# Kernel optimization log

Hardware: AMD Instinct MI355X
Metric: run time of the kernel (lower is better)

Reference implementation:

```python
import jax, jax.numpy as jnp
import numpy as np

B, C, H, W = 8, 64, 16, 16
TE = 128      # te_hidden
GT = 256      # rn_gt_hidden
FP = 256      # rn_fp_hidden
A = 32        # a_size
O = H * W
PAIR_IN = (C + 2) * 2 + TE  # 260, matches (cv_filter+2)*2 + te_hidden


def setup_inputs() -> dict:
    key = jax.random.key(0)
    ks = jax.random.split(key, 10)

    def w(k, fan_in, fan_out):
        return (jax.random.normal(k, (fan_in, fan_out), jnp.float32)
                / np.sqrt(fan_in).astype(np.float32))

    return {
        "x": jax.random.normal(ks[0], (B, C, H, W), jnp.float32),
        "code": jax.random.normal(ks[1], (B, TE), jnp.float32),
        "gt_w1": w(ks[2], PAIR_IN, GT), "gt_b1": jnp.zeros((GT,), jnp.float32),
        "gt_w2": w(ks[3], GT, GT),      "gt_b2": jnp.zeros((GT,), jnp.float32),
        "gt_w3": w(ks[4], GT, GT),      "gt_b3": jnp.zeros((GT,), jnp.float32),
        "fp_w1": w(ks[5], GT, FP),      "fp_b1": jnp.zeros((FP,), jnp.float32),
        "fp_w2": w(ks[6], FP, FP),      "fp_b2": jnp.zeros((FP,), jnp.float32),
        "fp_w3": w(ks[7], FP, A),       "fp_b3": jnp.zeros((A,), jnp.float32),
    }


def _coords(h, w):
    # 2 normalized coordinate channels in [-1, 1], one value per object
    ys = jnp.linspace(-1.0, 1.0, h, dtype=jnp.float32)
    xs = jnp.linspace(-1.0, 1.0, w, dtype=jnp.float32)
    yy, xx = jnp.meshgrid(ys, xs, indexing="ij")
    return jnp.stack([yy.ravel(), xx.ravel()], axis=-1)  # (o, 2)


def reference(x, code, gt_w1, gt_b1, gt_w2, gt_b2, gt_w3, gt_b3,
              fp_w1, fp_b1, fp_w2, fp_b2, fp_w3, fp_b3):
    b, c, h, w = x.shape
    o = h * w
    te = code.shape[-1]

    # rn_encode: flatten spatial grid to objects, append 2 coord channels
    xo = x.reshape(b, c, o).transpose(0, 2, 1)                 # (b, o, c)
    coord = jnp.broadcast_to(_coords(h, w)[None], (b, o, 2))
    xo = jnp.concatenate([xo, coord], axis=-1)                 # (b, o, c+2)

    # all O^2 ordered pairs + broadcast question code
    xi = jnp.broadcast_to(xo[:, :, None, :], (b, o, o, c + 2))
    xj = jnp.broadcast_to(xo[:, None, :, :], (b, o, o, c + 2))
    q = jnp.broadcast_to(code[:, None, None, :], (b, o, o, te))
    pairs = jnp.concatenate([xi, xj, q], axis=-1)              # (b, o, o, PAIR_IN)

    # g_theta MLP (ReLU after every layer)
    h1 = jax.nn.relu(pairs @ gt_w1 + gt_b1)
    h2 = jax.nn.relu(h1 @ gt_w2 + gt_b2)
    rel = jax.nn.relu(h2 @ gt_w3 + gt_b3)                      # (b, o, o, GT)

    # lower_sum: sum relations over the lower-triangular (i >= j) pairs
    mask = jnp.tril(jnp.ones((o, o), rel.dtype))
    summed = jnp.einsum("bijd,ij->bd", rel, mask)              # (b, GT)

    # f_phi MLP; no activation on final logits, dropout=0 (eval)
    f1 = jax.nn.relu(summed @ fp_w1 + fp_b1)
    f2 = jax.nn.relu(f1 @ fp_w2 + fp_b2)
    logits = f2 @ fp_w3 + fp_b3                                # (b, A)
    return logits
```

## Files before the change

kernel.cpp:

```cpp
#include <hip/hip_runtime.h>
#include <stdint.h>


#define NPAIR 32896

using short8  = __attribute__((ext_vector_type(8))) short;
using float4v = __attribute__((ext_vector_type(4))) float;

__device__ __forceinline__ float asf(unsigned u) {
    union { unsigned u; float f; } c; c.u = u; return c.f;
}
__device__ __forceinline__ unsigned short f2bf(float f) {
    union { float f; unsigned u; } c; c.f = f;
    unsigned u = c.u;
    u += 0x7FFFu + ((u >> 16) & 1u);
    return (unsigned short)(u >> 16);
}
__device__ __forceinline__ unsigned cvtpk(float lo, float hi) {
    unsigned r;
    asm("v_cvt_pk_bf16_f32 %0, %1, %2" : "=v"(r) : "v"(lo), "v"(hi));
    return r;
}
__device__ __forceinline__ void ij_of(int p, int& i, int& j) {
    float s = sqrtf(8.0f * (float)p + 1.0f);
    i = (int)((s - 1.0f) * 0.5f);
    while ((i + 1) * (i + 2) / 2 <= p) ++i;
    while (i * (i + 1) / 2 > p) --i;
    j = p - i * (i + 1) / 2;
}
__device__ __forceinline__ short8 buildA(uint4 uu, uint4 vv) {
    unsigned ua[4] = {uu.x, uu.y, uu.z, uu.w};
    unsigned va[4] = {vv.x, vv.y, vv.z, vv.w};
    union { unsigned u[4]; short8 s; } c;
    #pragma unroll
    for (int q = 0; q < 4; ++q) {
        float lo = asf(ua[q] << 16)         + asf(va[q] << 16);
        float hi = asf(ua[q] & 0xFFFF0000u) + asf(va[q] & 0xFFFF0000u);
        c.u[q] = cvtpk(fmaxf(lo, 0.f), fmaxf(hi, 0.f));
    }
    return c.s;
}

__global__ __launch_bounds__(256) void k_pre(
    const float* __restrict__ x, const float* __restrict__ code,
    const float* __restrict__ w1, const float* __restrict__ b1,
    const float* __restrict__ w2, const float* __restrict__ w3,
    unsigned short* __restrict__ ub, unsigned short* __restrict__ vb,
    unsigned short* __restrict__ w2t, unsigned short* __restrict__ w3t,
    float* __restrict__ summed)
{
    const int tid = threadIdx.x;
    if (blockIdx.x < 32) {
        const int ig = blockIdx.x, b = blockIdx.y, d = tid;
        float q = b1[d];
        const float* cp = code + b * 128;
        #pragma unroll 16
        for (int t = 0; t < 128; ++t) q += cp[t] * w1[(132 + t) * 256 + d];
        float su[8], sv[8];
        #pragma unroll
        for (int k = 0; k < 8; ++k) { su[k] = q; sv[k] = 0.f; }
        const float* xp = x + (b * 64) * 256 + ig * 8;
        #pragma unroll 8
        for (int c = 0; c < 64; ++c) {
            const float wu = w1[c * 256 + d];
            const float wv = w1[(66 + c) * 256 + d];
            const float* xc = xp + c * 256;
            #pragma unroll
            for (int k = 0; k < 8; ++k) { su[k] += xc[k] * wu; sv[k] += xc[k] * wv; }
        }
        const float wyu = w1[64 * 256 + d],  wxu = w1[65 * 256 + d];
        const float wyv = w1[130 * 256 + d], wxv = w1[131 * 256 + d];
        #pragma unroll
        for (int k = 0; k < 8; ++k) {
            const int i = ig * 8 + k;
            const float yy = (float)(i >> 4) * (2.0f / 15.0f) - 1.0f;
            const float xx = (float)(i & 15) * (2.0f / 15.0f) - 1.0f;
            ub[(b * 256 + i) * 256 + d] = f2bf(su[k] + yy * wyu + xx * wxu);
            vb[(b * 256 + i) * 256 + d] = f2bf(sv[k] + yy * wyv + xx * wxv);
        }
    } else {
        __shared__ float t[64][65];
        const int y = blockIdx.y;
        summed[y * 256 + tid] = 0.f;
        const int tx = tid & 63, ty = tid >> 6;
        for (int jj = 0; jj < 4; ++jj) {
            const int job = y * 4 + jj;
            const float* src = (job & 16) ? w3 : w2;
            unsigned short* dst = (job & 16) ? w3t : w2t;
            const int k0 = ((job >> 2) & 3) * 64, n0 = (job & 3) * 64;
            __syncthreads();
            #pragma unroll
            for (int r = ty; r < 64; r += 4) t[r][tx] = src[(k0 + r) * 256 + n0 + tx];
            __syncthreads();
            #pragma unroll
            for (int r = ty; r < 64; r += 4) dst[(n0 + r) * 256 + k0 + tx] = f2bf(t[tx][r]);
        }
    }
}

__global__ __launch_bounds__(512) void k_fuse(
    const unsigned short* __restrict__ ub, const unsigned short* __restrict__ vb,
    const unsigned short* __restrict__ w2t, const unsigned short* __restrict__ w3t,
    const float* __restrict__ b2, const float* __restrict__ b3,
    float* __restrict__ summed)
{
    extern __shared__ unsigned short lds[];
    const int tid  = threadIdx.x;
    const int pt   = blockIdx.x, b = blockIdx.y;
    const int lane = tid & 63, w = tid >> 6;
    const int lm   = lane & 15, quad = lane >> 4;

    #pragma unroll
    for (int it = 0; it < 16; ++it) {
        const int idx = it * 512 + tid;
        const int n = idx >> 5, c = idx & 31;
        const uint4 d = *(const uint4*)(w2t + n * 256 + c * 8);
        *(uint4*)(&lds[n * 256 + ((c ^ (n & 7)) << 3)]) = d;
    }

    const unsigned short* up[2];
    const unsigned short* vp[2];
    #pragma unroll
    for (int mt = 0; mt < 2; ++mt) {
        const int p = pt * 256 + w * 32 + mt * 16 + lm;
        int i, j; ij_of(p, i, j);
        up[mt] = ub + ((b * 256 + i) * 256) + quad * 8;
        vp[mt] = vb + ((b * 256 + j) * 256) + quad * 8;
    }
    __syncthreads();

    const float4v zero4 = {0.f, 0.f, 0.f, 0.f};

    float4v acc1[16][2];
    #pragma unroll
    for (int nt = 0; nt < 16; ++nt)
        #pragma unroll
        for (int mt = 0; mt < 2; ++mt) acc1[nt][mt] = zero4;
    {
        uint4 cu[3][2], cv[3][2];
        #pragma unroll
        for (int kk = 0; kk < 3; ++kk)
            #pragma unroll
            for (int mt = 0; mt < 2; ++mt) {
                cu[kk][mt] = *(const uint4*)(up[mt] + kk * 32);
                cv[kk][mt] = *(const uint4*)(vp[mt] + kk * 32);
            }
        #pragma unroll
        for (int ks = 0; ks < 8; ++ks) {
            const int pr = ks % 3;
            short8 afr[2];
            #pragma unroll
            for (int mt = 0; mt < 2; ++mt) afr[mt] = buildA(cu[pr][mt], cv[pr][mt]);
            if (ks < 5) {
                #pragma unroll
                for (int mt = 0; mt < 2; ++mt) {
                    cu[pr][mt] = *(const uint4*)(up[mt] + (ks + 3) * 32);
                    cv[pr][mt] = *(const uint4*)(vp[mt] + (ks + 3) * 32);
                }
            }
            const int coff = ((ks * 4 + quad) ^ (lm & 7)) << 3;
            __builtin_amdgcn_s_setprio(1);
            #pragma unroll
            for (int ng = 0; ng < 4; ++ng) {
                short8 bfr[4];
                #pragma unroll
                for (int q = 0; q < 4; ++q)
                    bfr[q] = *(const short8*)(&lds[((ng * 4 + q) * 16 + lm) * 256 + coff]);
                #pragma unroll
                for (int q = 0; q < 4; ++q)
                    #pragma unroll
                    for (int mt = 0; mt < 2; ++mt)
                        acc1[ng * 4 + q][mt] = __builtin_amdgcn_mfma_f32_16x16x32_bf16(
                            bfr[q], afr[mt], acc1[ng * 4 + q][mt], 0, 0, 0);
            }
            __builtin_amdgcn_s_setprio(0);
        }
    }
    __syncthreads();

    const unsigned short* bb3 = w3t + ((w * 32 + lm) * 256) + quad * 8;
    short8 bbuf[2][2];
    #pragma unroll
    for (int kk = 0; kk < 2; ++kk)
        #pragma unroll
        for (int nt = 0; nt < 2; ++nt)
            bbuf[kk][nt] = *(const short8*)(bb3 + nt * 4096 + kk * 32);

    #pragma unroll
    for (int nt = 0; nt < 16; ++nt) {
        const float4 bbv = *(const float4*)(b2 + nt * 16 + quad * 4);
        #pragma unroll
        for (int mt = 0; mt < 2; ++mt) {
            const int row = w * 32 + mt * 16 + lm;
            const float v0 = fmaxf(acc1[nt][mt][0] + bbv.x, 0.f);
            const float v1 = fmaxf(acc1[nt][mt][1] + bbv.y, 0.f);
            const float v2 = fmaxf(acc1[nt][mt][2] + bbv.z, 0.f);
            const float v3 = fmaxf(acc1[nt][mt][3] + bbv.w, 0.f);
            uint2 pk; pk.x = cvtpk(v0, v1); pk.y = cvtpk(v2, v3);
            const int c0 = nt * 2 + (quad >> 1);
            *(uint2*)(&lds[row * 256 + (((c0 ^ (row & 7)) << 3) | ((quad & 1) << 2))]) = pk;
        }
    }
    __syncthreads();

    float4v acc2[16][2];
    #pragma unroll
    for (int mt = 0; mt < 16; ++mt)
        #pragma unroll
        for (int nt = 0; nt < 2; ++nt) acc2[mt][nt] = zero4;
    {
        for (int ks = 0; ks < 8; ++ks) {
            const int pr = ks & 1;
            short8 bcur[2];
            #pragma unroll
            for (int nt = 0; nt < 2; ++nt) bcur[nt] = bbuf[pr][nt];
            if (ks < 6) {
                #pragma unroll
                for (int nt = 0; nt < 2; ++nt)
                    bbuf[pr][nt] = *(const short8*)(bb3 + nt * 4096 + (ks + 2) * 32);
            }
            __builtin_amdgcn_s_setprio(1);
            #pragma unroll
            for (int mt = 0; mt < 16; ++mt) {
                const int row = mt * 16 + lm;
                const short8 a = *(const short8*)(
                    &lds[row * 256 + (((ks * 4 + quad) ^ (row & 7)) << 3)]);
                #pragma unroll
                for (int nt = 0; nt < 2; ++nt)
                    acc2[mt][nt] = __builtin_amdgcn_mfma_f32_16x16x32_bf16(
                        a, bcur[nt], acc2[mt][nt], 0, 0, 0);
            }
            __builtin_amdgcn_s_setprio(0);
        }
    }

    #pragma unroll
    for (int nt = 0; nt < 2; ++nt) {
        const int col = w * 32 + nt * 16 + lm;
        const float bb = b3[col];
        float s = 0.f;
        #pragma unroll
        for (int mt = 0; mt < 16; ++mt)
            #pragma unroll
            for (int rg = 0; rg < 4; ++rg)
                s += fmaxf(acc2[mt][nt][rg] + bb, 0.f);
        s += __shfl_xor(s, 16);
        s += __shfl_xor(s, 32);
        if (quad == 0)
            atomicAdd(&summed[b * 256 + col], s);
    }
}

__global__ __launch_bounds__(1024) void k_tail(
    const unsigned short* __restrict__ ub, const unsigned short* __restrict__ vb,
    const unsigned short* __restrict__ w2t, const unsigned short* __restrict__ w3t,
    const float* __restrict__ b2, const float* __restrict__ b3,
    const float* __restrict__ summed,
    const float* __restrict__ fw1, const float* __restrict__ fb1,
    const float* __restrict__ fw2, const float* __restrict__ fb2,
    const float* __restrict__ fw3, const float* __restrict__ fb3,
    float* __restrict__ out)
{
    extern __shared__ unsigned short lds[];
    float* ext = (float*)(lds + 65536);
    float* s0  = ext + 256;
    float* s1  = s0 + 256;
    float* red = s1 + 256;
    const int b = blockIdx.x, tid = threadIdx.x;
    const int lane = tid & 63, w = tid >> 6;
    const int lm = lane & 15, quad = lane >> 4;
    const float4v zero4 = {0.f, 0.f, 0.f, 0.f};

    #pragma unroll
    for (int it = 0; it < 8; ++it) {
        const int idx = it * 1024 + tid;
        const int n = idx >> 5, c = idx & 31;
        const uint4 d4 = *(const uint4*)(w2t + n * 256 + c * 8);
        *(uint4*)(&lds[n * 256 + ((c ^ (n & 7)) << 3)]) = d4;
    }
    const int pp = 32768 + w * 16 + lm;
    const int p  = pp < NPAIR ? pp : NPAIR - 1;
    int i, j; ij_of(p, i, j);
    const unsigned short* up = ub + ((b * 256 + i) * 256) + quad * 8;
    const unsigned short* vp = vb + ((b * 256 + j) * 256) + quad * 8;
    __syncthreads();

    float4v acc1[16];
    #pragma unroll
    for (int nt = 0; nt < 16; ++nt) acc1[nt] = zero4;
    if (tid < 512) {
        #pragma unroll
        for (int ks = 0; ks < 8; ++ks) {
            const uint4 cu = *(const uint4*)(up + ks * 32);
            const uint4 cv = *(const uint4*)(vp + ks * 32);
            const short8 afr = buildA(cu, cv);
            const int coff = ((ks * 4 + quad) ^ (lm & 7)) << 3;
            #pragma unroll
            for (int nt = 0; nt < 16; ++nt) {
                const short8 bfr = *(const short8*)(&lds[(nt * 16 + lm) * 256 + coff]);
                acc1[nt] = __builtin_amdgcn_mfma_f32_16x16x32_bf16(
                    bfr, afr, acc1[nt], 0, 0, 0);
            }
        }
    }
    __syncthreads();

    if (tid < 512) {
        #pragma unroll
        for (int nt = 0; nt < 16; ++nt) {
            const float4 bbv = *(const float4*)(b2 + nt * 16 + quad * 4);
            const int row = w * 16 + lm;
            const float v0 = fmaxf(acc1[nt][0] + bbv.x, 0.f);
            const float v1 = fmaxf(acc1[nt][1] + bbv.y, 0.f);
            const float v2 = fmaxf(acc1[nt][2] + bbv.z, 0.f);
            const float v3 = fmaxf(acc1[nt][3] + bbv.w, 0.f);
            uint2 pk; pk.x = cvtpk(v0, v1); pk.y = cvtpk(v2, v3);
            const int c0 = nt * 2 + (quad >> 1);
            *(uint2*)(&lds[row * 256 + (((c0 ^ (row & 7)) << 3) | ((quad & 1) << 2))]) = pk;
        }
    }
    __syncthreads();

    float4v acc2[8][2];
    #pragma unroll
    for (int mt = 0; mt < 8; ++mt)
        #pragma unroll
        for (int nt = 0; nt < 2; ++nt) acc2[mt][nt] = zero4;
    if (tid < 512) {
        const unsigned short* bb3 = w3t + ((w * 32 + lm) * 256) + quad * 8;
        #pragma unroll
        for (int ks = 0; ks < 8; ++ks) {
            short8 bcur[2];
            #pragma unroll
            for (int nt = 0; nt < 2; ++nt)
                bcur[nt] = *(const short8*)(bb3 + nt * 4096 + ks * 32);
            const int coff = ((ks * 4 + quad) ^ (lm & 7)) << 3;
            #pragma unroll
            for (int mt = 0; mt < 8; ++mt) {
                const int row = mt * 16 + lm;
                const short8 a = *(const short8*)(
                    &lds[row * 256 + (((ks * 4 + quad) ^ (row & 7)) << 3)]);
                #pragma unroll
                for (int nt = 0; nt < 2; ++nt)
                    acc2[mt][nt] = __builtin_amdgcn_mfma_f32_16x16x32_bf16(
                        a, bcur[nt], acc2[mt][nt], 0, 0, 0);
            }
        }
        #pragma unroll
        for (int nt = 0; nt < 2; ++nt) {
            const int col = w * 32 + nt * 16 + lm;
            const float bb = b3[col];
            float s = 0.f;
            #pragma unroll
            for (int mt = 0; mt < 8; ++mt)
                #pragma unroll
                for (int rg = 0; rg < 4; ++rg)
                    s += fmaxf(acc2[mt][nt][rg] + bb, 0.f);
            s += __shfl_xor(s, 16);
            s += __shfl_xor(s, 32);
            if (quad == 0) ext[col] = s;
        }
    }
    __syncthreads();

    const int d = tid & 255, kh = tid >> 8;
    if (tid < 256) s0[tid] = summed[b * 256 + tid] + ext[tid];
    __syncthreads();
    float pk = 0.f;
    #pragma unroll 16
    for (int k = kh * 64; k < kh * 64 + 64; ++k) pk += s0[k] * fw1[k * 256 + d];
    red[kh * 256 + d] = pk;
    __syncthreads();
    if (tid < 256)
        s1[tid] = fmaxf(red[tid] + red[256 + tid] + red[512 + tid] + red[768 + tid]
                        + fb1[tid], 0.f);
    __syncthreads();
    pk = 0.f;
    #pragma unroll 16
    for (int k = kh * 64; k < kh * 64 + 64; ++k) pk += s1[k] * fw2[k * 256 + d];
    red[kh * 256 + d] = pk;
    __syncthreads();
    if (tid < 256)
        s0[tid] = fmaxf(red[tid] + red[256 + tid] + red[512 + tid] + red[768 + tid]
                        + fb2[tid], 0.f);
    __syncthreads();
    const int d3 = tid & 31, kh3 = tid >> 5;
    pk = 0.f;
    #pragma unroll
    for (int k = kh3 * 8; k < kh3 * 8 + 8; ++k) pk += s0[k] * fw3[k * 32 + d3];
    red[kh3 * 32 + d3] = pk;
    __syncthreads();
    if (tid < 32) {
        float o = fb3[tid];
        #pragma unroll 8
        for (int r = 0; r < 32; ++r) o += red[r * 32 + tid];
        out[b * 32 + tid] = o;
    }
}

extern "C" void kernel_launch(void* const* d_in, const int* in_sizes, int n_in,
                              void* d_out, int out_size, void* d_ws, size_t ws_size,
                              hipStream_t stream) {
    const float* x    = (const float*)d_in[0];
    const float* code = (const float*)d_in[1];
    const float* gw1  = (const float*)d_in[2];
    const float* gb1  = (const float*)d_in[3];
    const float* gw2  = (const float*)d_in[4];
    const float* gb2  = (const float*)d_in[5];
    const float* gw3  = (const float*)d_in[6];
    const float* gb3  = (const float*)d_in[7];
    const float* fw1  = (const float*)d_in[8];
    const float* fb1  = (const float*)d_in[9];
    const float* fw2  = (const float*)d_in[10];
    const float* fb2  = (const float*)d_in[11];
    const float* fw3  = (const float*)d_in[12];
    const float* fb3  = (const float*)d_in[13];
    float* out = (float*)d_out;

    char* ws = (char*)d_ws;
    unsigned short* ub  = (unsigned short*)(ws);
    unsigned short* vb  = (unsigned short*)(ws + 1048576);
    unsigned short* w2t = (unsigned short*)(ws + 2097152);
    unsigned short* w3t = (unsigned short*)(ws + 2228224);
    float* summed = (float*)(ws + 2359296);

    hipLaunchKernelGGL(k_pre, dim3(33, 8), dim3(256), 0, stream,
                       x, code, gw1, gb1, gw2, gw3, ub, vb, w2t, w3t, summed);
    hipLaunchKernelGGL(k_fuse, dim3(128, 8), dim3(512), 131072, stream,
                       ub, vb, w2t, w3t, gb2, gb3, summed);
    hipLaunchKernelGGL(k_tail, dim3(8), dim3(1024), 138240, stream,
                       ub, vb, w2t, w3t, gb2, gb3, summed,
                       fw1, fb1, fw2, fb2, fw3, fb3, out);
}
```

Baseline: 187.7 us.

## Stage built pair activations in LDS and use 2x4 warp tiling for both GEMMs

Layer-1 pair activations (relu(u_i+v_j)) are now built once per block and written to swizzled LDS, instead of being recomputed in registers per warp. W2 is no longer staged in LDS; its fragments are streamed from global memory with double buffering, as W3 already was. Warps are arranged as a 2x4 grid (128 rows by 64 columns per warp) for both the layer-2 and layer-3 MFMA GEMMs. This raises fragment reuse in registers and cuts LDS traffic per MFMA, at the cost of more global/L2 reads of weights per block and different register pressure. An unused coff variable is removed from k_tail.

```diff
diff --git a/kernel.cpp b/kernel.cpp
--- a/kernel.cpp
+++ b/kernel.cpp
@@ -39,6 +39,11 @@
         c.u[q] = cvtpk(fmaxf(lo, 0.f), fmaxf(hi, 0.f));
     }
     return c.s;
+}
+__device__ __forceinline__ uint4 build4(uint4 uu, uint4 vv) {
+    union { uint4 v; short8 s; } c;
+    c.s = buildA(uu, vv);
+    return c.v;
 }
 
 __global__ __launch_bounds__(256) void k_pre(
@@ -108,125 +113,119 @@
     const int tid  = threadIdx.x;
     const int pt   = blockIdx.x, b = blockIdx.y;
     const int lane = tid & 63, w = tid >> 6;
+    const int wm   = w >> 2, wn = w & 3;
     const int lm   = lane & 15, quad = lane >> 4;
 
-    #pragma unroll
-    for (int it = 0; it < 16; ++it) {
-        const int idx = it * 512 + tid;
-        const int n = idx >> 5, c = idx & 31;
-        const uint4 d = *(const uint4*)(w2t + n * 256 + c * 8);
-        *(uint4*)(&lds[n * 256 + ((c ^ (n & 7)) << 3)]) = d;
-    }
-
-    const unsigned short* up[2];
-    const unsigned short* vp[2];
-    #pragma unroll
-    for (int mt = 0; mt < 2; ++mt) {
-        const int p = pt * 256 + w * 32 + mt * 16 + lm;
+    const unsigned short* bb2 = w2t + ((wn * 64 + lm) * 256) + quad * 8;
+    const unsigned short* bb3 = w3t + ((wn * 64 + lm) * 256) + quad * 8;
+
+    short8 bbuf[2][4];
+    #pragma unroll
+    for (int kk = 0; kk < 2; ++kk)
+        #pragma unroll
+        for (int nt = 0; nt < 4; ++nt)
+            bbuf[kk][nt] = *(const short8*)(bb2 + nt * 4096 + kk * 32);
+
+    {
+        const int r = tid >> 1, half = tid & 1;
+        const int p = pt * 256 + r;
         int i, j; ij_of(p, i, j);
-        up[mt] = ub + ((b * 256 + i) * 256) + quad * 8;
-        vp[mt] = vb + ((b * 256 + j) * 256) + quad * 8;
+        const unsigned short* up = ub + ((b * 256 + i) * 256) + half * 128;
+        const unsigned short* vp = vb + ((b * 256 + j) * 256) + half * 128;
+        const int rs = r & 7;
+        #pragma unroll
+        for (int it = 0; it < 16; ++it) {
+            const uint4 uu = *(const uint4*)(up + it * 8);
+            const uint4 vv = *(const uint4*)(vp + it * 8);
+            const uint4 r4 = build4(uu, vv);
+            const int chunk = half * 16 + it;
+            *(uint4*)(&lds[r * 256 + ((chunk ^ rs) << 3)]) = r4;
+        }
     }
     __syncthreads();
 
     const float4v zero4 = {0.f, 0.f, 0.f, 0.f};
 
-    float4v acc1[16][2];
-    #pragma unroll
-    for (int nt = 0; nt < 16; ++nt)
-        #pragma unroll
-        for (int mt = 0; mt < 2; ++mt) acc1[nt][mt] = zero4;
+    float4v acc1[4][8];
+    #pragma unroll
+    for (int nt = 0; nt < 4; ++nt)
+        #pragma unroll
+        for (int mt = 0; mt < 8; ++mt) acc1[nt][mt] = zero4;
     {
-        uint4 cu[3][2], cv[3][2];
-        #pragma unroll
-        for (int kk = 0; kk < 3; ++kk)
-            #pragma unroll
-            for (int mt = 0; mt < 2; ++mt) {
-                cu[kk][mt] = *(const uint4*)(up[mt] + kk * 32);
-                cv[kk][mt] = *(const uint4*)(vp[mt] + kk * 32);
-            }
-        #pragma unroll
         for (int ks = 0; ks < 8; ++ks) {
-            const int pr = ks % 3;
-            short8 afr[2];
-            #pragma unroll
-            for (int mt = 0; mt < 2; ++mt) afr[mt] = buildA(cu[pr][mt], cv[pr][mt]);
-            if (ks < 5) {
-                #pragma unroll
-                for (int mt = 0; mt < 2; ++mt) {
-                    cu[pr][mt] = *(const uint4*)(up[mt] + (ks + 3) * 32);
-                    cv[pr][mt] = *(const uint4*)(vp[mt] + (ks + 3) * 32);
-                }
+            const int pr = ks & 1;
+            short8 bcur[4];
+            #pragma unroll
+            for (int nt = 0; nt < 4; ++nt) bcur[nt] = bbuf[pr][nt];
+            if (ks < 6) {
+                #pragma unroll
+                for (int nt = 0; nt < 4; ++nt)
+                    bbuf[pr][nt] = *(const short8*)(bb2 + nt * 4096 + (ks + 2) * 32);
             }
             const int coff = ((ks * 4 + quad) ^ (lm & 7)) << 3;
             __builtin_amdgcn_s_setprio(1);
             #pragma unroll
-            for (int ng = 0; ng < 4; ++ng) {
-                short8 bfr[4];
-                #pragma unroll
-                for (int q = 0; q < 4; ++q)
-                    bfr[q] = *(const short8*)(&lds[((ng * 4 + q) * 16 + lm) * 256 + coff]);
-                #pragma unroll
-                for (int q = 0; q < 4; ++q)
-                    #pragma unroll
-                    for (int mt = 0; mt < 2; ++mt)
-                        acc1[ng * 4 + q][mt] = __builtin_amdgcn_mfma_f32_16x16x32_bf16(
-                            bfr[q], afr[mt], acc1[ng * 4 + q][mt], 0, 0, 0);
+            for (int mt = 0; mt < 8; ++mt) {
+                const short8 afr = *(const short8*)(
+                    &lds[(wm * 128 + mt * 16 + lm) * 256 + coff]);
+                #pragma unroll
+                for (int nt = 0; nt < 4; ++nt)
+                    acc1[nt][mt] = __builtin_amdgcn_mfma_f32_16x16x32_bf16(
+                        bcur[nt], afr, acc1[nt][mt], 0, 0, 0);
             }
             __builtin_amdgcn_s_setprio(0);
         }
     }
     __syncthreads();
 
-    const unsigned short* bb3 = w3t + ((w * 32 + lm) * 256) + quad * 8;
-    short8 bbuf[2][2];
     #pragma unroll
     for (int kk = 0; kk < 2; ++kk)
         #pragma unroll
-        for (int nt = 0; nt < 2; ++nt)
+        for (int nt = 0; nt < 4; ++nt)
             bbuf[kk][nt] = *(const short8*)(bb3 + nt * 4096 + kk * 32);
 
     #pragma unroll
-    for (int nt = 0; nt < 16; ++nt) {
-        const float4 bbv = *(const float4*)(b2 + nt * 16 + quad * 4);
-        #pragma unroll
-        for (int mt = 0; mt < 2; ++mt) {
-            const int row = w * 32 + mt * 16 + lm;
+    for (int nt = 0; nt < 4; ++nt) {
+        const float4 bbv = *(const float4*)(b2 + wn * 64 + nt * 16 + quad * 4);
+        #pragma unroll
+        for (int mt = 0; mt < 8; ++mt) {
+            const int row = wm * 128 + mt * 16 + lm;
             const float v0 = fmaxf(acc1[nt][mt][0] + bbv.x, 0.f);
             const float v1 = fmaxf(acc1[nt][mt][1] + bbv.y, 0.f);
             const float v2 = fmaxf(acc1[nt][mt][2] + bbv.z, 0.f);
             const float v3 = fmaxf(acc1[nt][mt][3] + bbv.w, 0.f);
             uint2 pk; pk.x = cvtpk(v0, v1); pk.y = cvtpk(v2, v3);
-            const int c0 = nt * 2 + (quad >> 1);
-            *(uint2*)(&lds[row * 256 + (((c0 ^ (row & 7)) << 3) | ((quad & 1) << 2))]) = pk;
-        }
-    }
-    __syncthreads();
-
-    float4v acc2[16][2];
-    #pragma unroll
-    for (int mt = 0; mt < 16; ++mt)
-        #pragma unroll
-        for (int nt = 0; nt < 2; ++nt) acc2[mt][nt] = zero4;
+            const int c0 = wn * 8 + nt * 2 + (quad >> 1);
+            *(uint2*)(&lds[row * 256 +
+                           (((c0 ^ (row & 7)) << 3) | ((quad & 1) << 2))]) = pk;
+        }
+    }
+    __syncthreads();
+
+    float4v acc2[8][4];
+    #pragma unroll
+    for (int mt = 0; mt < 8; ++mt)
+        #pragma unroll
+        for (int nt = 0; nt < 4; ++nt) acc2[mt][nt] = zero4;
     {
         for (int ks = 0; ks < 8; ++ks) {
             const int pr = ks & 1;
-            short8 bcur[2];
-            #pragma unroll
-            for (int nt = 0; nt < 2; ++nt) bcur[nt] = bbuf[pr][nt];
+            short8 bcur[4];
+            #pragma unroll
+            for (int nt = 0; nt < 4; ++nt) bcur[nt] = bbuf[pr][nt];
             if (ks < 6) {
                 #pragma unroll
-                for (int nt = 0; nt < 2; ++nt)
+                for (int nt = 0; nt < 4; ++nt)
                     bbuf[pr][nt] = *(const short8*)(bb3 + nt * 4096 + (ks + 2) * 32);
             }
+            const int coff = ((ks * 4 + quad) ^ (lm & 7)) << 3;
             __builtin_amdgcn_s_setprio(1);
             #pragma unroll
-            for (int mt = 0; mt < 16; ++mt) {
-                const int row = mt * 16 + lm;
+            for (int mt = 0; mt < 8; ++mt) {
                 const short8 a = *(const short8*)(
-                    &lds[row * 256 + (((ks * 4 + quad) ^ (row & 7)) << 3)]);
-                #pragma unroll
-                for (int nt = 0; nt < 2; ++nt)
+                    &lds[(wm * 128 + mt * 16 + lm) * 256 + coff]);
+                #pragma unroll
+                for (int nt = 0; nt < 4; ++nt)
                     acc2[mt][nt] = __builtin_amdgcn_mfma_f32_16x16x32_bf16(
                         a, bcur[nt], acc2[mt][nt], 0, 0, 0);
             }
@@ -235,12 +234,12 @@
     }
 
     #pragma unroll
-    for (int nt = 0; nt < 2; ++nt) {
-        const int col = w * 32 + nt * 16 + lm;
+    for (int nt = 0; nt < 4; ++nt) {
+        const int col = wn * 64 + nt * 16 + lm;
         const float bb = b3[col];
         float s = 0.f;
         #pragma unroll
-        for (int mt = 0; mt < 16; ++mt)
+        for (int mt = 0; mt < 8; ++mt)
             #pragma unroll
             for (int rg = 0; rg < 4; ++rg)
                 s += fmaxf(acc2[mt][nt][rg] + bb, 0.f);
@@ -334,7 +333,6 @@
             #pragma unroll
             for (int nt = 0; nt < 2; ++nt)
                 bcur[nt] = *(const short8*)(bb3 + nt * 4096 + ks * 32);
-            const int coff = ((ks * 4 + quad) ^ (lm & 7)) << 3;
             #pragma unroll
             for (int mt = 0; mt < 8; ++mt) {
                 const int row = mt * 16 + lm;
```

New measurement: 221.6 us. +18.1%, slower.

## Restructure k_tail tail-pair MLP to use all 16 waves with pair/column tiling

Applied to the files above, without the earlier changes.

The tail kernel's 128 leftover pairs were handled by only 8 of 16 waves, each computing full 256-wide layer-2 outputs from an LDS-staged copy of w2. Now all 16 waves split the work into 4 pair groups by 4 column groups. The first-layer activations are built once into LDS, and w2/w3 fragments are streamed from global memory with a two-deep register prefetch instead of being copied into LDS. Layer-3 column sums are merged across pair groups with LDS atomics, which adds atomic contention and more global weight reads per wave in exchange for more parallelism and a removed staging copy.

```diff
diff --git a/kernel.cpp b/kernel.cpp
--- a/kernel.cpp
+++ b/kernel.cpp
@@ -39,6 +39,11 @@
         c.u[q] = cvtpk(fmaxf(lo, 0.f), fmaxf(hi, 0.f));
     }
     return c.s;
+}
+__device__ __forceinline__ uint4 build4(uint4 uu, uint4 vv) {
+    union { uint4 v; short8 s; } c;
+    c.s = buildA(uu, vv);
+    return c.v;
 }
 
 __global__ __launch_bounds__(256) void k_pre(
@@ -262,6 +267,8 @@
     float* __restrict__ out)
 {
     extern __shared__ unsigned short lds[];
+    unsigned short* h1t = lds;
+    unsigned short* h2t = lds + 32768;
     float* ext = (float*)(lds + 65536);
     float* s0  = ext + 256;
     float* s1  = s0 + 256;
@@ -269,97 +276,134 @@
     const int b = blockIdx.x, tid = threadIdx.x;
     const int lane = tid & 63, w = tid >> 6;
     const int lm = lane & 15, quad = lane >> 4;
+    const int pg = w >> 2, cg = w & 3;
     const float4v zero4 = {0.f, 0.f, 0.f, 0.f};
 
-    #pragma unroll
-    for (int it = 0; it < 8; ++it) {
-        const int idx = it * 1024 + tid;
-        const int n = idx >> 5, c = idx & 31;
-        const uint4 d4 = *(const uint4*)(w2t + n * 256 + c * 8);
-        *(uint4*)(&lds[n * 256 + ((c ^ (n & 7)) << 3)]) = d4;
-    }
-    const int pp = 32768 + w * 16 + lm;
-    const int p  = pp < NPAIR ? pp : NPAIR - 1;
-    int i, j; ij_of(p, i, j);
-    const unsigned short* up = ub + ((b * 256 + i) * 256) + quad * 8;
-    const unsigned short* vp = vb + ((b * 256 + j) * 256) + quad * 8;
-    __syncthreads();
-
-    float4v acc1[16];
-    #pragma unroll
-    for (int nt = 0; nt < 16; ++nt) acc1[nt] = zero4;
-    if (tid < 512) {
-        #pragma unroll
-        for (int ks = 0; ks < 8; ++ks) {
-            const uint4 cu = *(const uint4*)(up + ks * 32);
-            const uint4 cv = *(const uint4*)(vp + ks * 32);
-            const short8 afr = buildA(cu, cv);
-            const int coff = ((ks * 4 + quad) ^ (lm & 7)) << 3;
-            #pragma unroll
-            for (int nt = 0; nt < 16; ++nt) {
-                const short8 bfr = *(const short8*)(&lds[(nt * 16 + lm) * 256 + coff]);
-                acc1[nt] = __builtin_amdgcn_mfma_f32_16x16x32_bf16(
-                    bfr, afr, acc1[nt], 0, 0, 0);
-            }
-        }
-    }
-    __syncthreads();
-
-    if (tid < 512) {
-        #pragma unroll
-        for (int nt = 0; nt < 16; ++nt) {
-            const float4 bbv = *(const float4*)(b2 + nt * 16 + quad * 4);
-            const int row = w * 16 + lm;
-            const float v0 = fmaxf(acc1[nt][0] + bbv.x, 0.f);
-            const float v1 = fmaxf(acc1[nt][1] + bbv.y, 0.f);
-            const float v2 = fmaxf(acc1[nt][2] + bbv.z, 0.f);
-            const float v3 = fmaxf(acc1[nt][3] + bbv.w, 0.f);
+    if (tid < 256) ext[tid] = 0.f;
+
+    {
+        const int r = tid >> 3, q8 = tid & 7;
+        int i, j; ij_of(32768 + r, i, j);
+        const unsigned short* up = ub + ((b * 256 + i) * 256) + q8 * 32;
+        const unsigned short* vp = vb + ((b * 256 + j) * 256) + q8 * 32;
+        const int rs = r & 7;
+        #pragma unroll
+        for (int it = 0; it < 4; ++it) {
+            const uint4 uu = *(const uint4*)(up + it * 8);
+            const uint4 vv = *(const uint4*)(vp + it * 8);
+            const uint4 r4 = build4(uu, vv);
+            const int chunk = q8 * 4 + it;
+            *(uint4*)(&h1t[r * 256 + ((chunk ^ rs) << 3)]) = r4;
+        }
+    }
+    const unsigned short* bb2 = w2t + ((cg * 64 + lm) * 256) + quad * 8;
+    const unsigned short* bb3 = w3t + ((cg * 64 + lm) * 256) + quad * 8;
+    short8 bbuf[2][4];
+    #pragma unroll
+    for (int kk = 0; kk < 2; ++kk)
+        #pragma unroll
+        for (int nt = 0; nt < 4; ++nt)
+            bbuf[kk][nt] = *(const short8*)(bb2 + nt * 4096 + kk * 32);
+    __syncthreads();
+
+    float4v acc[4][2];
+    #pragma unroll
+    for (int nt = 0; nt < 4; ++nt)
+        #pragma unroll
+        for (int mt = 0; mt < 2; ++mt) acc[nt][mt] = zero4;
+    #pragma unroll
+    for (int ks = 0; ks < 8; ++ks) {
+        const int pr = ks & 1;
+        short8 bcur[4];
+        #pragma unroll
+        for (int nt = 0; nt < 4; ++nt) bcur[nt] = bbuf[pr][nt];
+        if (ks < 6) {
+            #pragma unroll
+            for (int nt = 0; nt < 4; ++nt)
+                bbuf[pr][nt] = *(const short8*)(bb2 + nt * 4096 + (ks + 2) * 32);
+        }
+        const int coff = ((ks * 4 + quad) ^ (lm & 7)) << 3;
+        short8 afr[2];
+        #pragma unroll
+        for (int mt = 0; mt < 2; ++mt)
+            afr[mt] = *(const short8*)(&h1t[(pg * 32 + mt * 16 + lm) * 256 + coff]);
+        #pragma unroll
+        for (int nt = 0; nt < 4; ++nt)
+            #pragma unroll
+            for (int mt = 0; mt < 2; ++mt)
+                acc[nt][mt] = __builtin_amdgcn_mfma_f32_16x16x32_bf16(
+                    bcur[nt], afr[mt], acc[nt][mt], 0, 0, 0);
+    }
+
+    #pragma unroll
+    for (int kk = 0; kk < 2; ++kk)
+        #pragma unroll
+        for (int nt = 0; nt < 4; ++nt)
+            bbuf[kk][nt] = *(const short8*)(bb3 + nt * 4096 + kk * 32);
+
+    #pragma unroll
+    for (int nt = 0; nt < 4; ++nt) {
+        const float4 bbv = *(const float4*)(b2 + cg * 64 + nt * 16 + quad * 4);
+        #pragma unroll
+        for (int mt = 0; mt < 2; ++mt) {
+            const int row = pg * 32 + mt * 16 + lm;
+            const float v0 = fmaxf(acc[nt][mt][0] + bbv.x, 0.f);
+            const float v1 = fmaxf(acc[nt][mt][1] + bbv.y, 0.f);
+            const float v2 = fmaxf(acc[nt][mt][2] + bbv.z, 0.f);
+            const float v3 = fmaxf(acc[nt][mt][3] + bbv.w, 0.f);
             uint2 pk; pk.x = cvtpk(v0, v1); pk.y = cvtpk(v2, v3);
-            const int c0 = nt * 2 + (quad >> 1);
-            *(uint2*)(&lds[row * 256 + (((c0 ^ (row & 7)) << 3) | ((quad & 1) << 2))]) = pk;
-        }
-    }
-    __syncthreads();
-
-    float4v acc2[8][2];
-    #pragma unroll
-    for (int mt = 0; mt < 8; ++mt)
-        #pragma unroll
-        for (int nt = 0; nt < 2; ++nt) acc2[mt][nt] = zero4;
-    if (tid < 512) {
-        const unsigned short* bb3 = w3t + ((w * 32 + lm) * 256) + quad * 8;
-        #pragma unroll
-        for (int ks = 0; ks < 8; ++ks) {
-            short8 bcur[2];
-            #pragma unroll
-            for (int nt = 0; nt < 2; ++nt)
-                bcur[nt] = *(const short8*)(bb3 + nt * 4096 + ks * 32);
-            const int coff = ((ks * 4 + quad) ^ (lm & 7)) << 3;
-            #pragma unroll
-            for (int mt = 0; mt < 8; ++mt) {
-                const int row = mt * 16 + lm;
-                const short8 a = *(const short8*)(
-                    &lds[row * 256 + (((ks * 4 + quad) ^ (row & 7)) << 3)]);
-                #pragma unroll
-                for (int nt = 0; nt < 2; ++nt)
-                    acc2[mt][nt] = __builtin_amdgcn_mfma_f32_16x16x32_bf16(
-                        a, bcur[nt], acc2[mt][nt], 0, 0, 0);
-            }
-        }
-        #pragma unroll
-        for (int nt = 0; nt < 2; ++nt) {
-            const int col = w * 32 + nt * 16 + lm;
-            const float bb = b3[col];
-            float s = 0.f;
-            #pragma unroll
-            for (int mt = 0; mt < 8; ++mt)
-                #pragma unroll
-                for (int rg = 0; rg < 4; ++rg)
-                    s += fmaxf(acc2[mt][nt][rg] + bb, 0.f);
-            s += __shfl_xor(s, 16);
-            s += __shfl_xor(s, 32);
-            if (quad == 0) ext[col] = s;
-        }
+            const int c0 = cg * 8 + nt * 2 + (quad >> 1);
+            *(uint2*)(&h2t[row * 256 +
+                           (((c0 ^ (row & 7)) << 3) | ((quad & 1) << 2))]) = pk;
+        }
+    }
+    __syncthreads();
+
+    float4v acc2[2][4];
+    #pragma unroll
+    for (int mt = 0; mt < 2; ++mt)
+        #pragma unroll
+        for (int nt = 0; nt < 4; ++nt) acc2[mt][nt] = zero4;
+    #pragma unroll
+    for (int ks = 0; ks < 8; ++ks) {
+        const int pr = ks & 1;
+        short8 bcur[4];
+        #pragma unroll
+        for (int nt = 0; nt < 4; ++nt) bcur[nt] = bbuf[pr][nt];
+        if (ks < 6) {
+            #pragma unroll
+            for (int nt = 0; nt < 4; ++nt)
+                bbuf[pr][nt] = *(const short8*)(bb3 + nt * 4096 + (ks + 2) * 32);
+        }
+        const int coff = ((ks * 4 + quad) ^ (lm & 7)) << 3;
+        short8 afr[2];
+        #pragma unroll
+        for (int mt = 0; mt < 2; ++mt) {
+            const int row = pg * 32 + mt * 16 + lm;
+            afr[mt] = *(const short8*)(&h2t[row * 256 + coff]);
+        }
+        #pragma unroll
+        for (int mt = 0; mt < 2; ++mt)
+            #pragma unroll
+            for (int nt = 0; nt < 4; ++nt)
+                acc2[mt][nt] = __builtin_amdgcn_mfma_f32_16x16x32_bf16(
+                    afr[mt], bcur[nt], acc2[mt][nt], 0, 0, 0);
+    }
+
+    #pragma unroll
+    for (int nt = 0; nt < 4; ++nt) {
+        const int col = cg * 64 + nt * 16 + lm;
+        const float bb = b3[col];
+        float s = 0.f;
+        #pragma unroll
+        for (int mt = 0; mt < 2; ++mt)
+            #pragma unroll
+            for (int rg = 0; rg < 4; ++rg)
+                s += fmaxf(acc2[mt][nt][rg] + bb, 0.f);
+        s += __shfl_xor(s, 16);
+        s += __shfl_xor(s, 32);
+        if (quad == 0)
+            atomicAdd(&ext[col], s);
     }
     __syncthreads();
 
```

New measurement: 205.7 us (median of 2 runs). 9.6% more time.
